# Kernel optimization log

Hardware: AMD Instinct MI355X
Metric: run time of the kernel (lower is better)

## Reference

```python
import jax, jax.numpy as jnp
import numpy as np

N = 50000   # nodes
E = 800000  # edges
F = 256     # feature dim (in = hidden = out)
L = 3       # number_layers


def _arma_conv(x, src, dst, w, Wi, Wr, b):
    # GCN normalization without self loops (PyG ARMAConv default)
    deg = jax.ops.segment_sum(w, dst, num_segments=N)                 # [N]
    dinv = jnp.where(deg > 0, jax.lax.rsqrt(deg), 0.0)
    norm = dinv[src] * w * dinv[dst]                                   # [E]
    h = x @ Wi                                                         # [N, F]
    agg = jax.ops.segment_sum(norm[:, None] * h[src], dst, num_segments=N)  # [N, F]
    # root dropout is inactive in eval mode
    return jax.nn.relu(agg + x @ Wr + b)


def setup_inputs() -> dict:
    key = jax.random.key(0)
    ks = jax.random.split(key, 6)
    x = jax.random.normal(ks[0], (N, F), jnp.float32)
    edge_index = jax.random.randint(ks[1], (2, E), 0, N, jnp.int32)
    edge_attr = jax.random.uniform(ks[2], (E,), jnp.float32)
    s = 1.0 / np.sqrt(F)
    W_init = jax.random.normal(ks[3], (L, F, F), jnp.float32) * s
    W_root = jax.random.normal(ks[4], (L, F, F), jnp.float32) * s
    bias = jnp.zeros((L, F), jnp.float32)
    return dict(x=x, edge_index=edge_index, edge_attr=edge_attr,
                W_init=W_init, W_root=W_root, bias=bias)


def reference(x, edge_index, edge_attr, W_init, W_root, bias):
    src, dst = edge_index[0], edge_index[1]
    for i in range(L):  # fixed small layer count
        x = _arma_conv(x, src, dst, edge_attr, W_init[i], W_root[i], bias[i])
        # outer functional.relu is a no-op after the conv's internal ReLU;
        # dropout is inactive in eval mode.
    return x
```

## Files before the change

kernel.cpp:

```cpp
#include <hip/hip_runtime.h>
#include <hip/hip_bf16.h>

#define N_NODES 50000
#define N_EDGES 800000
#define FDIM 256
#define N_LAYERS 3
#define NB_SCAN ((N_NODES + 255) / 256)

typedef __attribute__((ext_vector_type(8))) short bf16x8;
typedef __attribute__((ext_vector_type(8))) unsigned short u16x8;
typedef __attribute__((ext_vector_type(4))) float f32x4;

__device__ inline unsigned short f2bf(float f) {
  unsigned int u = __float_as_uint(f);
  unsigned int r = u + 0x7FFFu + ((u >> 16) & 1u);
  return (unsigned short)(r >> 16);
}
__device__ inline float bf2f(unsigned short s) {
  return __uint_as_float(((unsigned int)s) << 16);
}
__device__ inline void split2(float f, unsigned short& h, unsigned short& l) {
  h = f2bf(f);
  l = f2bf(f - bf2f(h));
}

#define GLOAD16(g, l) __builtin_amdgcn_global_load_lds( \
    (const __attribute__((address_space(1))) void*)(g), \
    (__attribute__((address_space(3))) void*)(l), 16, 0, 0)


__global__ void deg_count_kernel(const int* __restrict__ dst,
                                 const float* __restrict__ w,
                                 float* __restrict__ deg,
                                 int* __restrict__ cnt, int E) {
  int e = blockIdx.x * blockDim.x + threadIdx.x;
  if (e < E) {
    int d = dst[e];
    atomicAdd(&deg[d], w[e]);
    atomicAdd(&cnt[d], 1);
  }
}

__global__ void dinv_kernel(const float* __restrict__ deg,
                            float* __restrict__ dinv, int n) {
  int i = blockIdx.x * blockDim.x + threadIdx.x;
  if (i < n) {
    float d = deg[i];
    dinv[i] = (d > 0.f) ? (1.f / sqrtf(d)) : 0.f;
  }
}

__global__ __launch_bounds__(256)
void blocksum_kernel(const int* __restrict__ cnt, int* __restrict__ bsum, int n) {
  int b = blockIdx.x;
  int t = threadIdx.x;
  int i = b * 256 + t;
  int v = (i < n) ? cnt[i] : 0;
  #pragma unroll
  for (int d = 1; d < 64; d <<= 1) v += __shfl_xor(v, d, 64);
  __shared__ int ws[4];
  if ((t & 63) == 0) ws[t >> 6] = v;
  __syncthreads();
  if (t == 0) bsum[b] = ws[0] + ws[1] + ws[2] + ws[3];
}

__global__ __launch_bounds__(256)
void scanb_kernel(const int* __restrict__ bsum, int* __restrict__ bpre,
                  int* __restrict__ offs_end) {
  int t = threadIdx.x;
  int lane = t & 63, wid = t >> 6;
  int v = (t < NB_SCAN) ? bsum[t] : 0;
  int incl = v;
  #pragma unroll
  for (int d = 1; d < 64; d <<= 1) {
    int tmp = __shfl_up(incl, d, 64);
    if (lane >= d) incl += tmp;
  }
  __shared__ int wsum[4];
  if (lane == 63) wsum[wid] = incl;
  __syncthreads();
  if (t == 0) {
    int s = 0;
    #pragma unroll
    for (int k = 0; k < 4; ++k) { int tt = wsum[k]; wsum[k] = s; s += tt; }
  }
  __syncthreads();
  int excl = incl - v + wsum[wid];
  if (t < NB_SCAN) bpre[t] = excl;
  if (t == NB_SCAN - 1) *offs_end = excl + v;
}

__global__ __launch_bounds__(256)
void offs_kernel(const int* __restrict__ cnt, const int* __restrict__ bpre,
                 int* __restrict__ offs, int* __restrict__ cursor, int n) {
  int b = blockIdx.x;
  int t = threadIdx.x;
  int lane = t & 63, wid = t >> 6;
  int i = b * 256 + t;
  int v = (i < n) ? cnt[i] : 0;
  int incl = v;
  #pragma unroll
  for (int d = 1; d < 64; d <<= 1) {
    int tmp = __shfl_up(incl, d, 64);
    if (lane >= d) incl += tmp;
  }
  __shared__ int wsum[4];
  if (lane == 63) wsum[wid] = incl;
  __syncthreads();
  if (t == 0) {
    int s = 0;
    #pragma unroll
    for (int k = 0; k < 4; ++k) { int tt = wsum[k]; wsum[k] = s; s += tt; }
  }
  __syncthreads();
  int excl = incl - v + wsum[wid] + bpre[b];
  if (i < n) { offs[i] = excl; cursor[i] = excl; }
}

__global__ void scatter_kernel(const int* __restrict__ src,
                               const int* __restrict__ dst,
                               const float* __restrict__ w,
                               const float* __restrict__ dinv,
                               int* __restrict__ cursor,
                               int* __restrict__ src_s,
                               float* __restrict__ norm_s, int E) {
  int e = blockIdx.x * blockDim.x + threadIdx.x;
  if (e < E) {
    int s = src[e], d = dst[e];
    int pos = atomicAdd(&cursor[d], 1);
    src_s[pos] = s;
    norm_s[pos] = dinv[s] * w[e] * dinv[d];
  }
}

__global__ void split_kernel(const float* __restrict__ x,
                             unsigned short* __restrict__ xhi,
                             unsigned short* __restrict__ xlo, int n4) {
  int i = blockIdx.x * blockDim.x + threadIdx.x;
  if (i < n4) {
    float4 v = reinterpret_cast<const float4*>(x)[i];
    ushort4 h, l;
    split2(v.x, h.x, l.x);
    split2(v.y, h.y, l.y);
    split2(v.z, h.z, l.z);
    split2(v.w, h.w, l.w);
    reinterpret_cast<ushort4*>(xhi)[i] = h;
    reinterpret_cast<ushort4*>(xlo)[i] = l;
  }
}

__global__ __launch_bounds__(256)
void wsplit_kernel(const float* __restrict__ Wi_a,
                   const float* __restrict__ Wr_a,
                   unsigned short* __restrict__ wthi,
                   unsigned short* __restrict__ wtlo) {
  __shared__ float tile[32][33];
  int m6 = blockIdx.x >> 6;
  int tid = blockIdx.x & 63;
  int tk = (tid >> 3) * 32;
  int tn = (tid & 7) * 32;
  int layer = m6 >> 1;
  const float* W = ((m6 & 1) ? Wr_a : Wi_a) + (size_t)layer * FDIM * FDIM;
  int t = threadIdx.x;
  int lr = t >> 3;
  int lc = (t & 7) * 4;
  float4 v = *reinterpret_cast<const float4*>(W + (size_t)(tk + lr) * FDIM + tn + lc);
  tile[lr][lc + 0] = v.x; tile[lr][lc + 1] = v.y;
  tile[lr][lc + 2] = v.z; tile[lr][lc + 3] = v.w;
  __syncthreads();
  ushort4 h, l;
  split2(tile[lc + 0][lr], h.x, l.x);
  split2(tile[lc + 1][lr], h.y, l.y);
  split2(tile[lc + 2][lr], h.z, l.z);
  split2(tile[lc + 3][lr], h.w, l.w);
  size_t o = ((size_t)m6 * FDIM + tn + lr) * FDIM + tk + lc;
  *reinterpret_cast<ushort4*>(wthi + o) = h;
  *reinterpret_cast<ushort4*>(wtlo + o) = l;
}


__global__ __launch_bounds__(256)
void agg_kernel(const unsigned short* __restrict__ xh,
                const float* __restrict__ norm_s,
                const int* __restrict__ src_s,
                const int* __restrict__ offs,
                unsigned short* __restrict__ agh,
                unsigned short* __restrict__ agl, int n) {
  int t = threadIdx.x;
  int lane = t & 63;
  int node = blockIdx.x * 8 + ((t >> 6) << 1) + (lane >> 5);
  if (node >= n) return;
  int fl = lane & 31;
  int beg = offs[node];
  int end = offs[node + 1];
  float a[8];
  #pragma unroll
  for (int f = 0; f < 8; ++f) a[f] = 0.f;
  const unsigned short* xbase = xh + fl * 8;
  int j = beg;
  for (; j + 8 <= end; j += 8) {
    int sj[8];
    float wj[8];
    #pragma unroll
    for (int u = 0; u < 8; ++u) { sj[u] = src_s[j + u]; wj[u] = norm_s[j + u]; }
    u16x8 v[8];
    #pragma unroll
    for (int u = 0; u < 8; ++u)
      v[u] = *reinterpret_cast<const u16x8*>(xbase + (size_t)sj[u] * FDIM);
    #pragma unroll
    for (int u = 0; u < 8; ++u)
      #pragma unroll
      for (int f = 0; f < 8; ++f)
        a[f] += wj[u] * bf2f(v[u][f]);
  }
  for (; j < end; ++j) {
    int s = src_s[j];
    float wv = norm_s[j];
    u16x8 v = *reinterpret_cast<const u16x8*>(xbase + (size_t)s * FDIM);
    #pragma unroll
    for (int f = 0; f < 8; ++f) a[f] += wv * bf2f(v[f]);
  }
  u16x8 hh, ll;
  #pragma unroll
  for (int f = 0; f < 8; ++f) {
    unsigned short h, l;
    split2(a[f], h, l);
    hh[f] = h; ll[f] = l;
  }
  size_t base = (size_t)node * FDIM + fl * 8;
  *reinterpret_cast<u16x8*>(agh + base) = hh;
  *reinterpret_cast<u16x8*>(agl + base) = ll;
}


#define STAGE_TILE(TI, GPTR, ROWB, CLAMP, K0)                                     \
  {                                                                               \
    int s0_ = t;                                                                  \
    int rr_ = s0_ >> 2;                                                           \
    int sl_ = (s0_ & 3) ^ ((rr_ >> 1) & 3);                                       \
    int r2_ = (ROWB) + rr_; if (CLAMP && r2_ >= M) r2_ = M - 1;                   \
    GLOAD16((GPTR) + (size_t)r2_ * FDIM + (K0) + sl_ * 8,                         \
            smem + (TI) * 8192 + s0_ * 16);                                       \
    int s1_ = t + 256;                                                            \
    rr_ = s1_ >> 2;                                                               \
    sl_ = (s1_ & 3) ^ ((rr_ >> 1) & 3);                                           \
    r2_ = (ROWB) + rr_; if (CLAMP && r2_ >= M) r2_ = M - 1;                       \
    GLOAD16((GPTR) + (size_t)r2_ * FDIM + (K0) + sl_ * 8,                         \
            smem + (TI) * 8192 + s1_ * 16);                                       \
  }

#define STAGE_ALL(K0)                      \
  STAGE_TILE(0, agh, rowBase, 1, K0);      \
  STAGE_TILE(1, agl, rowBase, 1, K0);      \
  STAGE_TILE(2, xh, rowBase, 1, K0);       \
  STAGE_TILE(3, xl, rowBase, 1, K0);       \
  STAGE_TILE(4, wih, nBase, 0, K0);        \
  STAGE_TILE(5, wil, nBase, 0, K0);        \
  STAGE_TILE(6, wrh, nBase, 0, K0);        \
  STAGE_TILE(7, wrl, nBase, 0, K0);

__global__ __launch_bounds__(256, 2)
void gemm_dual_kernel(const unsigned short* __restrict__ agh,
                      const unsigned short* __restrict__ agl,
                      const unsigned short* __restrict__ xh,
                      const unsigned short* __restrict__ xl,
                      const unsigned short* __restrict__ wih,
                      const unsigned short* __restrict__ wil,
                      const unsigned short* __restrict__ wrh,
                      const unsigned short* __restrict__ wrl,
                      const float* __restrict__ bias,
                      unsigned short* __restrict__ oh,
                      unsigned short* __restrict__ ol,
                      float* __restrict__ ofinal,
                      int writeFinal, int M) {
  __shared__ __align__(16) unsigned char smem[65536];
  const int t = threadIdx.x;
  const int lane = t & 63;
  const int w = t >> 6;

  const int nwg = gridDim.x;
  const int bq = nwg >> 3, br = nwg & 7;
  const int xcd = blockIdx.x & 7;
  const int idx = blockIdx.x >> 3;
  const int wgid = (xcd < br ? xcd * (bq + 1) : br * (bq + 1) + (xcd - br) * bq) + idx;
  const int rowBase = (wgid >> 1) * 128;
  const int nBase = (wgid & 1) * 128;

  const int wm = (w >> 1) * 64;
  const int wn = (w & 1) * 64;

  f32x4 acc[4][4];
  #pragma unroll
  for (int i = 0; i < 4; ++i)
    #pragma unroll
    for (int j = 0; j < 4; ++j)
      acc[i][j] = (f32x4)(0.f);

  STAGE_ALL(0);

  for (int s = 0; s < 8; ++s) {
    __syncthreads();

    const int q = lane >> 4;
    bf16x8 fah[4], fal[4], fxh[4], fxl[4];
    bf16x8 bih[4], bil[4], brh[4], brl[4];
    #pragma unroll
    for (int i = 0; i < 4; ++i) {
      int R = wm + i * 16 + (lane & 15);
      int offA = R * 64 + ((q ^ ((R >> 1) & 3)) * 16);
      fah[i] = *reinterpret_cast<const bf16x8*>(smem + offA);
      fal[i] = *reinterpret_cast<const bf16x8*>(smem + 8192 + offA);
      fxh[i] = *reinterpret_cast<const bf16x8*>(smem + 16384 + offA);
      fxl[i] = *reinterpret_cast<const bf16x8*>(smem + 24576 + offA);
      int Rb = wn + i * 16 + (lane & 15);
      int offB = Rb * 64 + ((q ^ ((Rb >> 1) & 3)) * 16);
      bih[i] = *reinterpret_cast<const bf16x8*>(smem + 32768 + offB);
      bil[i] = *reinterpret_cast<const bf16x8*>(smem + 40960 + offB);
      brh[i] = *reinterpret_cast<const bf16x8*>(smem + 49152 + offB);
      brl[i] = *reinterpret_cast<const bf16x8*>(smem + 57344 + offB);
    }
    asm volatile("s_waitcnt lgkmcnt(0)" ::: "memory");
    __builtin_amdgcn_sched_barrier(0);
    __builtin_amdgcn_s_barrier();
    __builtin_amdgcn_sched_barrier(0);

    if (s < 7) {
      int k1 = (s + 1) * 32;
      STAGE_ALL(k1);
    }

    #pragma unroll
    for (int j = 0; j < 4; ++j) {
      #pragma unroll
      for (int i = 0; i < 4; ++i) {
        acc[i][j] = __builtin_amdgcn_mfma_f32_16x16x32_bf16(fal[i], bih[j], acc[i][j], 0, 0, 0);
        acc[i][j] = __builtin_amdgcn_mfma_f32_16x16x32_bf16(fah[i], bil[j], acc[i][j], 0, 0, 0);
        acc[i][j] = __builtin_amdgcn_mfma_f32_16x16x32_bf16(fah[i], bih[j], acc[i][j], 0, 0, 0);
        acc[i][j] = __builtin_amdgcn_mfma_f32_16x16x32_bf16(fxl[i], brh[j], acc[i][j], 0, 0, 0);
        acc[i][j] = __builtin_amdgcn_mfma_f32_16x16x32_bf16(fxh[i], brl[j], acc[i][j], 0, 0, 0);
        acc[i][j] = __builtin_amdgcn_mfma_f32_16x16x32_bf16(fxh[i], brh[j], acc[i][j], 0, 0, 0);
      }
    }
  }

  const int cr = lane & 15;
  const int r4 = (lane >> 4) * 4;
  #pragma unroll
  for (int i = 0; i < 4; ++i)
    #pragma unroll
    for (int j = 0; j < 4; ++j) {
      int col = nBase + wn + j * 16 + cr;
      float badd = bias[col];
      #pragma unroll
      for (int e = 0; e < 4; ++e) {
        int row = rowBase + wm + i * 16 + r4 + e;
        if (row < M) {
          float val = fmaxf(acc[i][j][e] + badd, 0.f);
          size_t o = (size_t)row * FDIM + col;
          if (writeFinal) {
            ofinal[o] = val;
          } else {
            unsigned short hh, ll;
            split2(val, hh, ll);
            oh[o] = hh;
            ol[o] = ll;
          }
        }
      }
    }
}


extern "C" void kernel_launch(void* const* d_in, const int* in_sizes, int n_in,
                              void* d_out, int out_size, void* d_ws, size_t ws_size,
                              hipStream_t stream) {
  (void)in_sizes; (void)n_in; (void)out_size; (void)ws_size;
  const float* x0   = (const float*)d_in[0];
  const int*   ei   = (const int*)d_in[1];
  const float* ea   = (const float*)d_in[2];
  const float* Wi_a = (const float*)d_in[3];
  const float* Wr_a = (const float*)d_in[4];
  const float* b_a  = (const float*)d_in[5];
  float* out = (float*)d_out;

  const int* src = ei;
  const int* dst = ei + N_EDGES;

  char* ws = (char*)d_ws;
  size_t off = 0;
  auto alloc = [&](size_t bytes) {
    char* p = ws + off;
    off += (bytes + 255) & ~(size_t)255;
    return p;
  };
  const size_t NF2 = (size_t)N_NODES * FDIM * 2;
  unsigned short* XAh = (unsigned short*)alloc(NF2);
  unsigned short* XAl = (unsigned short*)alloc(NF2);
  unsigned short* XBh = (unsigned short*)alloc(NF2);
  unsigned short* XBl = (unsigned short*)alloc(NF2);
  unsigned short* agh = (unsigned short*)alloc(NF2);
  unsigned short* agl = (unsigned short*)alloc(NF2);
  unsigned short* wthi = (unsigned short*)alloc((size_t)N_LAYERS * 2 * FDIM * FDIM * 2);
  unsigned short* wtlo = (unsigned short*)alloc((size_t)N_LAYERS * 2 * FDIM * FDIM * 2);
  float* deg    = (float*)alloc((size_t)N_NODES * 4);
  float* dinv   = (float*)alloc((size_t)N_NODES * 4);
  int*   cnt    = (int*)alloc((size_t)N_NODES * 4);
  int*   offs   = (int*)alloc((size_t)(N_NODES + 1) * 4);
  int*   cursor = (int*)alloc((size_t)N_NODES * 4);
  int*   src_s  = (int*)alloc((size_t)N_EDGES * 4);
  float* norm_s = (float*)alloc((size_t)N_EDGES * 4);
  int*   bsum   = (int*)alloc((size_t)NB_SCAN * 4);
  int*   bpre   = (int*)alloc((size_t)NB_SCAN * 4);

  hipMemsetAsync(deg, 0, (size_t)N_NODES * 4, stream);
  hipMemsetAsync(cnt, 0, (size_t)N_NODES * 4, stream);

  deg_count_kernel<<<(N_EDGES + 255) / 256, 256, 0, stream>>>(dst, ea, deg, cnt, N_EDGES);
  dinv_kernel<<<(N_NODES + 255) / 256, 256, 0, stream>>>(deg, dinv, N_NODES);
  blocksum_kernel<<<NB_SCAN, 256, 0, stream>>>(cnt, bsum, N_NODES);
  scanb_kernel<<<1, 256, 0, stream>>>(bsum, bpre, offs + N_NODES);
  offs_kernel<<<NB_SCAN, 256, 0, stream>>>(cnt, bpre, offs, cursor, N_NODES);
  scatter_kernel<<<(N_EDGES + 255) / 256, 256, 0, stream>>>(src, dst, ea, dinv, cursor,
                                                            src_s, norm_s, N_EDGES);
  wsplit_kernel<<<6 * 64, 256, 0, stream>>>(Wi_a, Wr_a, wthi, wtlo);
  int n4 = N_NODES * FDIM / 4;
  split_kernel<<<(n4 + 255) / 256, 256, 0, stream>>>(x0, XAh, XAl, n4);

  const size_t WMAT = (size_t)FDIM * FDIM;
  int nrow = (N_NODES + 127) / 128;
  dim3 ggrid(nrow * 2);
  unsigned short* curh = XAh; unsigned short* curl = XAl;
  unsigned short* nxth = XBh; unsigned short* nxtl = XBl;
  for (int l = 0; l < N_LAYERS; ++l) {
    agg_kernel<<<(N_NODES + 7) / 8, 256, 0, stream>>>(curh, norm_s, src_s, offs,
                                                      agh, agl, N_NODES);
    int writeFinal = (l == N_LAYERS - 1) ? 1 : 0;
    gemm_dual_kernel<<<ggrid, 256, 0, stream>>>(
        agh, agl, curh, curl,
        wthi + (size_t)(l * 2) * WMAT, wtlo + (size_t)(l * 2) * WMAT,
        wthi + (size_t)(l * 2 + 1) * WMAT, wtlo + (size_t)(l * 2 + 1) * WMAT,
        b_a + (size_t)l * FDIM,
        nxth, nxtl, out, writeFinal, N_NODES);
    unsigned short* th = curh; unsigned short* tl = curl;
    curh = nxth; curl = nxtl; nxth = th; nxtl = tl;
  }
}
```

Before: 627.9 us.

## Enlarge GEMM tile to 256 rows with 512 threads; compute degree from sorted edges

The dual GEMM now uses 512-thread workgroups covering 256 rows by 128 columns. Each B (weight) tile staged in LDS is reused across twice as many rows, and LDS grows to 96KB. Separately, the float atomic degree accumulation is replaced by per-node sums over the CSR-sorted edge weights, and norm is computed in its own kernel. This removes the float atomics and makes the degree sum deterministic, at the cost of two extra small kernels and an extra edge-weight array.

```diff
diff --git a/kernel.cpp b/kernel.cpp
--- a/kernel.cpp
+++ b/kernel.cpp
@@ -30,24 +30,9 @@
 
 
 __global__ void deg_count_kernel(const int* __restrict__ dst,
-                                 const float* __restrict__ w,
-                                 float* __restrict__ deg,
                                  int* __restrict__ cnt, int E) {
   int e = blockIdx.x * blockDim.x + threadIdx.x;
-  if (e < E) {
-    int d = dst[e];
-    atomicAdd(&deg[d], w[e]);
-    atomicAdd(&cnt[d], 1);
-  }
-}
-
-__global__ void dinv_kernel(const float* __restrict__ deg,
-                            float* __restrict__ dinv, int n) {
-  int i = blockIdx.x * blockDim.x + threadIdx.x;
-  if (i < n) {
-    float d = deg[i];
-    dinv[i] = (d > 0.f) ? (1.f / sqrtf(d)) : 0.f;
-  }
+  if (e < E) atomicAdd(&cnt[dst[e]], 1);
 }
 
 __global__ __launch_bounds__(256)
@@ -120,16 +105,41 @@
 __global__ void scatter_kernel(const int* __restrict__ src,
                                const int* __restrict__ dst,
                                const float* __restrict__ w,
-                               const float* __restrict__ dinv,
                                int* __restrict__ cursor,
                                int* __restrict__ src_s,
-                               float* __restrict__ norm_s, int E) {
+                               float* __restrict__ w_s, int E) {
   int e = blockIdx.x * blockDim.x + threadIdx.x;
   if (e < E) {
-    int s = src[e], d = dst[e];
+    int d = dst[e];
     int pos = atomicAdd(&cursor[d], 1);
-    src_s[pos] = s;
-    norm_s[pos] = dinv[s] * w[e] * dinv[d];
+    src_s[pos] = src[e];
+    w_s[pos] = w[e];
+  }
+}
+
+__global__ void degdinv_kernel(const float* __restrict__ w_s,
+                               const int* __restrict__ offs,
+                               float* __restrict__ dinv, int n) {
+  int i = blockIdx.x * blockDim.x + threadIdx.x;
+  if (i < n) {
+    int beg = offs[i], end = offs[i + 1];
+    float s = 0.f;
+    for (int j = beg; j < end; ++j) s += w_s[j];
+    dinv[i] = (s > 0.f) ? (1.f / sqrtf(s)) : 0.f;
+  }
+}
+
+__global__ void norm_kernel(const float* __restrict__ w_s,
+                            const int* __restrict__ src_s,
+                            const int* __restrict__ offs,
+                            const float* __restrict__ dinv,
+                            float* __restrict__ norm_s, int n) {
+  int i = blockIdx.x * blockDim.x + threadIdx.x;
+  if (i < n) {
+    int beg = offs[i], end = offs[i + 1];
+    float dn = dinv[i];
+    for (int j = beg; j < end; ++j)
+      norm_s[j] = dinv[src_s[j]] * w_s[j] * dn;
   }
 }
 
@@ -233,33 +243,42 @@
 }
 
 
-#define STAGE_TILE(TI, GPTR, ROWB, CLAMP, K0)                                     \
+#define STAGE_A(TI, GPTR, K0)                                                     \
   {                                                                               \
     int s0_ = t;                                                                  \
     int rr_ = s0_ >> 2;                                                           \
     int sl_ = (s0_ & 3) ^ ((rr_ >> 1) & 3);                                       \
-    int r2_ = (ROWB) + rr_; if (CLAMP && r2_ >= M) r2_ = M - 1;                   \
+    int r2_ = rowBase + rr_; if (r2_ >= M) r2_ = M - 1;                           \
     GLOAD16((GPTR) + (size_t)r2_ * FDIM + (K0) + sl_ * 8,                         \
-            smem + (TI) * 8192 + s0_ * 16);                                       \
-    int s1_ = t + 256;                                                            \
+            smem + (TI) * 16384 + s0_ * 16);                                      \
+    int s1_ = t + 512;                                                            \
     rr_ = s1_ >> 2;                                                               \
     sl_ = (s1_ & 3) ^ ((rr_ >> 1) & 3);                                           \
-    r2_ = (ROWB) + rr_; if (CLAMP && r2_ >= M) r2_ = M - 1;                       \
+    r2_ = rowBase + rr_; if (r2_ >= M) r2_ = M - 1;                               \
     GLOAD16((GPTR) + (size_t)r2_ * FDIM + (K0) + sl_ * 8,                         \
-            smem + (TI) * 8192 + s1_ * 16);                                       \
+            smem + (TI) * 16384 + s1_ * 16);                                      \
+  }
+
+#define STAGE_B(TI, GPTR, K0)                                                     \
+  {                                                                               \
+    int s0_ = t;                                                                  \
+    int rr_ = s0_ >> 2;                                                           \
+    int sl_ = (s0_ & 3) ^ ((rr_ >> 1) & 3);                                       \
+    GLOAD16((GPTR) + (size_t)(nBase + rr_) * FDIM + (K0) + sl_ * 8,               \
+            smem + 65536 + (TI) * 8192 + s0_ * 16);                               \
   }
 
 #define STAGE_ALL(K0)                      \
-  STAGE_TILE(0, agh, rowBase, 1, K0);      \
-  STAGE_TILE(1, agl, rowBase, 1, K0);      \
-  STAGE_TILE(2, xh, rowBase, 1, K0);       \
-  STAGE_TILE(3, xl, rowBase, 1, K0);       \
-  STAGE_TILE(4, wih, nBase, 0, K0);        \
-  STAGE_TILE(5, wil, nBase, 0, K0);        \
-  STAGE_TILE(6, wrh, nBase, 0, K0);        \
-  STAGE_TILE(7, wrl, nBase, 0, K0);
-
-__global__ __launch_bounds__(256, 2)
+  STAGE_A(0, agh, K0);                     \
+  STAGE_A(1, agl, K0);                     \
+  STAGE_A(2, xh, K0);                      \
+  STAGE_A(3, xl, K0);                      \
+  STAGE_B(0, wih, K0);                     \
+  STAGE_B(1, wil, K0);                     \
+  STAGE_B(2, wrh, K0);                     \
+  STAGE_B(3, wrl, K0);
+
+__global__ __launch_bounds__(512, 2)
 void gemm_dual_kernel(const unsigned short* __restrict__ agh,
                       const unsigned short* __restrict__ agl,
                       const unsigned short* __restrict__ xh,
@@ -273,7 +292,7 @@
                       unsigned short* __restrict__ ol,
                       float* __restrict__ ofinal,
                       int writeFinal, int M) {
-  __shared__ __align__(16) unsigned char smem[65536];
+  __shared__ __align__(16) unsigned char smem[98304];
   const int t = threadIdx.x;
   const int lane = t & 63;
   const int w = t >> 6;
@@ -283,7 +302,7 @@
   const int xcd = blockIdx.x & 7;
   const int idx = blockIdx.x >> 3;
   const int wgid = (xcd < br ? xcd * (bq + 1) : br * (bq + 1) + (xcd - br) * bq) + idx;
-  const int rowBase = (wgid >> 1) * 128;
+  const int rowBase = (wgid >> 1) * 256;
   const int nBase = (wgid & 1) * 128;
 
   const int wm = (w >> 1) * 64;
@@ -309,15 +328,15 @@
       int R = wm + i * 16 + (lane & 15);
       int offA = R * 64 + ((q ^ ((R >> 1) & 3)) * 16);
       fah[i] = *reinterpret_cast<const bf16x8*>(smem + offA);
-      fal[i] = *reinterpret_cast<const bf16x8*>(smem + 8192 + offA);
-      fxh[i] = *reinterpret_cast<const bf16x8*>(smem + 16384 + offA);
-      fxl[i] = *reinterpret_cast<const bf16x8*>(smem + 24576 + offA);
+      fal[i] = *reinterpret_cast<const bf16x8*>(smem + 16384 + offA);
+      fxh[i] = *reinterpret_cast<const bf16x8*>(smem + 32768 + offA);
+      fxl[i] = *reinterpret_cast<const bf16x8*>(smem + 49152 + offA);
       int Rb = wn + i * 16 + (lane & 15);
-      int offB = Rb * 64 + ((q ^ ((Rb >> 1) & 3)) * 16);
-      bih[i] = *reinterpret_cast<const bf16x8*>(smem + 32768 + offB);
-      bil[i] = *reinterpret_cast<const bf16x8*>(smem + 40960 + offB);
-      brh[i] = *reinterpret_cast<const bf16x8*>(smem + 49152 + offB);
-      brl[i] = *reinterpret_cast<const bf16x8*>(smem + 57344 + offB);
+      int offB = 65536 + Rb * 64 + ((q ^ ((Rb >> 1) & 3)) * 16);
+      bih[i] = *reinterpret_cast<const bf16x8*>(smem + offB);
+      bil[i] = *reinterpret_cast<const bf16x8*>(smem + 8192 + offB);
+      brh[i] = *reinterpret_cast<const bf16x8*>(smem + 16384 + offB);
+      brl[i] = *reinterpret_cast<const bf16x8*>(smem + 24576 + offB);
     }
     asm volatile("s_waitcnt lgkmcnt(0)" ::: "memory");
     __builtin_amdgcn_sched_barrier(0);
@@ -402,32 +421,33 @@
   unsigned short* agl = (unsigned short*)alloc(NF2);
   unsigned short* wthi = (unsigned short*)alloc((size_t)N_LAYERS * 2 * FDIM * FDIM * 2);
   unsigned short* wtlo = (unsigned short*)alloc((size_t)N_LAYERS * 2 * FDIM * FDIM * 2);
-  float* deg    = (float*)alloc((size_t)N_NODES * 4);
   float* dinv   = (float*)alloc((size_t)N_NODES * 4);
   int*   cnt    = (int*)alloc((size_t)N_NODES * 4);
   int*   offs   = (int*)alloc((size_t)(N_NODES + 1) * 4);
   int*   cursor = (int*)alloc((size_t)N_NODES * 4);
   int*   src_s  = (int*)alloc((size_t)N_EDGES * 4);
+  float* w_s    = (float*)alloc((size_t)N_EDGES * 4);
   float* norm_s = (float*)alloc((size_t)N_EDGES * 4);
   int*   bsum   = (int*)alloc((size_t)NB_SCAN * 4);
   int*   bpre   = (int*)alloc((size_t)NB_SCAN * 4);
 
-  hipMemsetAsync(deg, 0, (size_t)N_NODES * 4, stream);
   hipMemsetAsync(cnt, 0, (size_t)N_NODES * 4, stream);
 
-  deg_count_kernel<<<(N_EDGES + 255) / 256, 256, 0, stream>>>(dst, ea, deg, cnt, N_EDGES);
-  dinv_kernel<<<(N_NODES + 255) / 256, 256, 0, stream>>>(deg, dinv, N_NODES);
+  deg_count_kernel<<<(N_EDGES + 255) / 256, 256, 0, stream>>>(dst, cnt, N_EDGES);
   blocksum_kernel<<<NB_SCAN, 256, 0, stream>>>(cnt, bsum, N_NODES);
   scanb_kernel<<<1, 256, 0, stream>>>(bsum, bpre, offs + N_NODES);
   offs_kernel<<<NB_SCAN, 256, 0, stream>>>(cnt, bpre, offs, cursor, N_NODES);
-  scatter_kernel<<<(N_EDGES + 255) / 256, 256, 0, stream>>>(src, dst, ea, dinv, cursor,
-                                                            src_s, norm_s, N_EDGES);
+  scatter_kernel<<<(N_EDGES + 255) / 256, 256, 0, stream>>>(src, dst, ea, cursor,
+                                                            src_s, w_s, N_EDGES);
+  degdinv_kernel<<<(N_NODES + 255) / 256, 256, 0, stream>>>(w_s, offs, dinv, N_NODES);
+  norm_kernel<<<(N_NODES + 255) / 256, 256, 0, stream>>>(w_s, src_s, offs, dinv,
+                                                         norm_s, N_NODES);
   wsplit_kernel<<<6 * 64, 256, 0, stream>>>(Wi_a, Wr_a, wthi, wtlo);
   int n4 = N_NODES * FDIM / 4;
   split_kernel<<<(n4 + 255) / 256, 256, 0, stream>>>(x0, XAh, XAl, n4);
 
   const size_t WMAT = (size_t)FDIM * FDIM;
-  int nrow = (N_NODES + 127) / 128;
+  int nrow = (N_NODES + 255) / 256;
   dim3 ggrid(nrow * 2);
   unsigned short* curh = XAh; unsigned short* curl = XAl;
   unsigned short* nxth = XBh; unsigned short* nxtl = XBl;
@@ -435,7 +455,7 @@
     agg_kernel<<<(N_NODES + 7) / 8, 256, 0, stream>>>(curh, norm_s, src_s, offs,
                                                       agh, agl, N_NODES);
     int writeFinal = (l == N_LAYERS - 1) ? 1 : 0;
-    gemm_dual_kernel<<<ggrid, 256, 0, stream>>>(
+    gemm_dual_kernel<<<ggrid, 512, 0, stream>>>(
         agh, agl, curh, curl,
         wthi + (size_t)(l * 2) * WMAT, wtlo + (size_t)(l * 2) * WMAT,
         wthi + (size_t)(l * 2 + 1) * WMAT, wtlo + (size_t)(l * 2 + 1) * WMAT,
```

Measured after the change: 600.8 us. 1.05x faster.
